# Kernel tuning notes

Measured on AMD Instinct MI355X. Metric: run time of the kernel, lower is better.

Reference implementation:

```python
import jax, jax.numpy as jnp
import numpy as np

H = 128          # hidden_dim
L = 3            # n_layers
G = 128          # num graphs in batch
BN_EPS = 1e-5


def setup_inputs() -> dict:
    key = jax.random.key(0)
    ks = jax.random.split(key, 16)
    N, E, ND, ED = 2048, 8192, 32, 16
    s = lambda k, shape, fan: jax.random.normal(k, shape, dtype=jnp.float32) / np.sqrt(fan)
    return {
        "x": jax.random.normal(ks[0], (N, ND), dtype=jnp.float32),
        "edge_index": jax.random.randint(ks[1], (2, E), 0, N),
        "edge_attr": jax.random.normal(ks[2], (E, ED), dtype=jnp.float32),
        "batch": jnp.sort(jax.random.randint(ks[3], (N,), 0, G)),
        "node_W": s(ks[4], (ND, H), ND),
        "node_b": jnp.zeros((H,), jnp.float32),
        "edge_W": s(ks[5], (L, ED, H * H), ED),
        "edge_b": jnp.zeros((L, H * H), jnp.float32),
        "root_W": s(ks[6], (L, H, H), H),
        "conv_bias": jnp.zeros((L, H), jnp.float32),
        "bn_gamma": jnp.ones((L, H), jnp.float32),
        "bn_beta": jnp.zeros((L, H), jnp.float32),
        "cls_W1": s(ks[7], (H, 64), H),
        "cls_b1": jnp.zeros((64,), jnp.float32),
        "cls_W2": s(ks[8], (64, 1), 64),
        "cls_b2": jnp.zeros((1,), jnp.float32),
    }


def _segment_mean(vals, ids, num_segments):
    ssum = jax.ops.segment_sum(vals, ids, num_segments=num_segments)
    cnt = jax.ops.segment_sum(jnp.ones((vals.shape[0],), vals.dtype), ids,
                              num_segments=num_segments)
    return ssum / jnp.maximum(cnt, 1.0)[:, None]


def reference(x, edge_index, edge_attr, batch, node_W, node_b, edge_W, edge_b,
              root_W, conv_bias, bn_gamma, bn_beta, cls_W1, cls_b1, cls_W2, cls_b2):
    N = x.shape[0]
    src, dst = edge_index[0], edge_index[1]
    h = x @ node_W + node_b                                   # [N, H]
    for l in range(L):
        # edge-conditioned weights: [E, H, H]
        W = (edge_attr @ edge_W[l] + edge_b[l]).reshape(-1, H, H)
        msg = jnp.einsum('ei,eio->eo', h[src], W)             # gather + per-edge matmul
        agg = _segment_mean(msg, dst, N)                      # scatter-mean
        x_new = h @ root_W[l] + agg + conv_bias[l]
        # BatchNorm (batch statistics, training-mode math)
        mu = jnp.mean(x_new, axis=0)
        var = jnp.var(x_new, axis=0)
        x_new = (x_new - mu) * jax.lax.rsqrt(var + BN_EPS) * bn_gamma[l] + bn_beta[l]
        x_new = jax.nn.relu(x_new)                            # dropout omitted (eval)
        h = h + x_new                                         # residual
    g = _segment_mean(h, batch, G)                            # global mean pool [G, H]
    out = jax.nn.relu(g @ cls_W1 + cls_b1) @ cls_W2 + cls_b2  # classifier
    return out.squeeze(-1)                                    # [G]
```

## Files before the change

kernel.cpp:

```cpp
#include <hip/hip_runtime.h>
#include <cstddef>
#include <cstdint>

#define H 128
#define EDIM 16
#define NLAYER 3
#define KU 2304
#define NSLICE 18
#define ASTRIDE 2312

typedef unsigned short ushort_t;
typedef unsigned int uint_t;
typedef __attribute__((ext_vector_type(8))) short bf16x8;
typedef __attribute__((ext_vector_type(4))) float f32x4;

__device__ __forceinline__ ushort_t f2bf(float f) {
    uint_t u = __builtin_bit_cast(uint_t, f);
    u += 0x7fffu + ((u >> 16) & 1u);
    return (ushort_t)(u >> 16);
}
__device__ __forceinline__ uint_t pack2(float a, float b) {
    return (uint_t)f2bf(a) | ((uint_t)f2bf(b) << 16);
}

__global__ __launch_bounds__(1024) void setup_kernel(
    const int* __restrict__ dst, const int* __restrict__ batch,
    const float* __restrict__ x, const float* __restrict__ node_W,
    const float* __restrict__ node_b,
    const float* __restrict__ eW, const float* __restrict__ eb,
    const float* __restrict__ rW,
    int* __restrict__ offs, int* __restrict__ deg, int* __restrict__ eord,
    float* __restrict__ cntG, float* __restrict__ bnS, float* __restrict__ bnQ,
    float* __restrict__ gsum, float* __restrict__ h, ushort_t* __restrict__ Wt2,
    int E, int N, int G)
{
    alignas(16) __shared__ unsigned char smem[36864];
    const int b = blockIdx.x;
    const int t = threadIdx.x;

    if (b == 0) {
        int* sh = (int*)smem;
        int* part = sh + 2048;
        for (int i = t; i < N; i += 1024) sh[i] = 0;
        __syncthreads();
        for (int e = t; e < E; e += 1024) atomicAdd(&sh[dst[e]], 1);
        __syncthreads();
        const int v0 = (2 * t < N) ? sh[2 * t] : 0;
        const int v1 = (2 * t + 1 < N) ? sh[2 * t + 1] : 0;
        part[t] = v0 + v1;
        __syncthreads();
        for (int off = 1; off < 1024; off <<= 1) {
            int xp = (t >= off) ? part[t - off] : 0;
            __syncthreads();
            part[t] += xp;
            __syncthreads();
        }
        const int boff = (t == 0) ? 0 : part[t - 1];
        if (2 * t < N) { deg[2 * t] = v0; offs[2 * t] = boff; }
        if (2 * t + 1 < N) { deg[2 * t + 1] = v1; offs[2 * t + 1] = boff + v0; }
        if (t == 1023) offs[N] = part[1023];
        __syncthreads();
        if (2 * t < N) sh[2 * t] = boff;
        if (2 * t + 1 < N) sh[2 * t + 1] = boff + v0;
        __syncthreads();
        for (int e = t; e < E; e += 1024) {
            const int d = dst[e];
            const int pos = atomicAdd(&sh[d], 1);
            eord[pos] = e;
        }
        return;
    }

    if (b <= NLAYER * NSLICE) {
        ushort_t* tile = (ushort_t*)smem;
        const int bb = b - 1;
        const int l = bb / NSLICE, s = bb % NSLICE;
        const float* S = (s < 16) ? (eW + ((size_t)l * 16 + s) * (H * H))
                       : (s == 16 ? (eb + (size_t)l * H * H)
                                  : (rW + (size_t)l * H * H));
        const int k = t >> 3, o0 = (t & 7) * 16;
#pragma unroll
        for (int j = 0; j < 16; j += 4) {
            float4 v = *(const float4*)&S[(size_t)k * H + o0 + j];
            tile[k * 136 + o0 + j + 0] = f2bf(v.x);
            tile[k * 136 + o0 + j + 1] = f2bf(v.y);
            tile[k * 136 + o0 + j + 2] = f2bf(v.z);
            tile[k * 136 + o0 + j + 3] = f2bf(v.w);
        }
        __syncthreads();
        const int n = t >> 3, k0 = (t & 7) * 16;
        ushort_t* outp = Wt2 + ((size_t)(l * H + n)) * KU + s * H + k0;
#pragma unroll
        for (int j = 0; j < 16; ++j) outp[j] = tile[(k0 + j) * 136 + n];
        return;
    }

    if (b <= NLAYER * NSLICE + 16) {
        const int sub = t >> 8;
        const int st = t & 255;
        float* As = (float*)(smem + sub * 8704);
        float* Bs = As + 16 * 68;
        const int tt = (b - (NLAYER * NSLICE + 1)) * 4 + sub;
        const int bm = (tt >> 1) * 64;
        const int bn = (tt & 1) * 64;
        const int tx = st & 15, ty = st >> 4;
        float acc[4][4];
#pragma unroll
        for (int i = 0; i < 4; ++i)
#pragma unroll
            for (int j = 0; j < 4; ++j) acc[i][j] = 0.f;
        const int ka = st & 15, ma = st >> 4;
        const int nb = st & 63, kb = st >> 6;
        for (int k0 = 0; k0 < 32; k0 += 16) {
#pragma unroll
            for (int r = 0; r < 4; ++r)
                As[ka * 68 + ma + 16 * r] = x[(size_t)(bm + ma + 16 * r) * 32 + (k0 + ka)];
#pragma unroll
            for (int r = 0; r < 4; ++r)
                Bs[(kb + 4 * r) * 68 + nb] = node_W[(size_t)(k0 + kb + 4 * r) * H + bn + nb];
            __syncthreads();
#pragma unroll
            for (int kk = 0; kk < 16; ++kk) {
                const float4 a4 = *(const float4*)&As[kk * 68 + ty * 4];
                const float4 b4 = *(const float4*)&Bs[kk * 68 + tx * 4];
                const float a[4] = {a4.x, a4.y, a4.z, a4.w};
                const float bv[4] = {b4.x, b4.y, b4.z, b4.w};
#pragma unroll
                for (int i = 0; i < 4; ++i)
#pragma unroll
                    for (int j = 0; j < 4; ++j)
                        acc[i][j] = fmaf(a[i], bv[j], acc[i][j]);
            }
            __syncthreads();
        }
#pragma unroll
        for (int i = 0; i < 4; ++i) {
            const int row = bm + ty * 4 + i;
            float4 v;
            v.x = acc[i][0] + node_b[bn + tx * 4 + 0];
            v.y = acc[i][1] + node_b[bn + tx * 4 + 1];
            v.z = acc[i][2] + node_b[bn + tx * 4 + 2];
            v.w = acc[i][3] + node_b[bn + tx * 4 + 3];
            *(float4*)&h[(size_t)row * H + bn + tx * 4] = v;
        }
        return;
    }

    {
        const int zcount = G * H + 2 * NLAYER * H + G;
        for (int i = t; i < zcount; i += 1024) {
            if (i < G * H) gsum[i] = 0.f;
            else if (i < G * H + NLAYER * H) bnS[i - G * H] = 0.f;
            else if (i < G * H + 2 * NLAYER * H) bnQ[i - G * H - NLAYER * H] = 0.f;
            else cntG[i - G * H - 2 * NLAYER * H] = 0.f;
        }
        __syncthreads();
        for (int v = t; v < N; v += 1024) atomicAdd(&cntG[batch[v]], 1.f);
    }
}

__global__ __launch_bounds__(512, 4) void ubuild_gemm(
    const float* __restrict__ h, const float* __restrict__ ea,
    const int* __restrict__ src, const int* __restrict__ offs,
    const int* __restrict__ deg, const int* __restrict__ eord,
    const ushort_t* __restrict__ Wt2l,
    float* __restrict__ xnew, float* __restrict__ bnS, float* __restrict__ bnQ)
{
    __shared__ ushort_t As8[8 * ASTRIDE];
    __shared__ ushort_t Bs[128][136];
    const int tid = threadIdx.x;
    const int w = tid >> 6;
    const int lane = tid & 63;
    const int m0 = blockIdx.x * 8;

    {
        const int v = m0 + w;
        const int j = lane;
        float u[17][2];
#pragma unroll
        for (int d = 0; d < 17; ++d) { u[d][0] = 0.f; u[d][1] = 0.f; }
        const int st = offs[v];
        const int dg = deg[v];
        for (int k = 0; k < dg; ++k) {
            const int e = eord[st + k];
            const int s = src[e];
            const float* eap = ea + (size_t)e * EDIM;
            const float4 w0 = *(const float4*)(eap + 0);
            const float4 w1 = *(const float4*)(eap + 4);
            const float4 w2 = *(const float4*)(eap + 8);
            const float4 w3 = *(const float4*)(eap + 12);
            const float wv[16] = {w0.x, w0.y, w0.z, w0.w, w1.x, w1.y, w1.z, w1.w,
                                  w2.x, w2.y, w2.z, w2.w, w3.x, w3.y, w3.z, w3.w};
            const float2 h2 = *(const float2*)&h[(size_t)s * H + 2 * j];
            u[16][0] += h2.x;
            u[16][1] += h2.y;
#pragma unroll
            for (int d = 0; d < 16; ++d) {
                u[d][0] = fmaf(wv[d], h2.x, u[d][0]);
                u[d][1] = fmaf(wv[d], h2.y, u[d][1]);
            }
        }
        const float rc = 1.0f / (float)(dg > 0 ? dg : 1);
        uint_t* urow = (uint_t*)&As8[w * ASTRIDE];
#pragma unroll
        for (int d = 0; d < 17; ++d)
            urow[j + d * 64] = pack2(u[d][0] * rc, u[d][1] * rc);
        const float2 hv = *(const float2*)&h[(size_t)v * H + 2 * j];
        urow[j + 17 * 64] = pack2(hv.x, hv.y);
    }

    const int l15 = lane & 15, quad = lane >> 4;
    f32x4 acc = {0.f, 0.f, 0.f, 0.f};
    const ushort_t* arow = &As8[(l15 & 7) * ASTRIDE];

    for (int c = 0; c < KU / 128; ++c) {
#pragma unroll
        for (int r = 0; r < 4; ++r) {
            const int idx = tid + r * 512;
            const int row = idx >> 4, pos = (idx & 15) * 8;
            *(uint4*)&Bs[row][pos] =
                *(const uint4*)&Wt2l[(size_t)row * KU + c * 128 + pos];
        }
        __syncthreads();
#pragma unroll
        for (int ks = 0; ks < 4; ++ks) {
            const int k = ks * 32 + quad * 8;
            bf16x8 a = *(const bf16x8*)&arow[c * 128 + k];
            bf16x8 b = *(const bf16x8*)&Bs[w * 16 + l15][k];
            acc = __builtin_amdgcn_mfma_f32_16x16x32_bf16(a, b, acc, 0, 0, 0);
        }
        __syncthreads();
    }

    const int col = w * 16 + l15;
    float s = 0.f, q = 0.f;
    if (quad < 2) {
#pragma unroll
        for (int r = 0; r < 4; ++r) {
            const int m = quad * 4 + r;
            const float val = acc[r];
            xnew[(size_t)(m0 + m) * H + col] = val;
            s += val;
            q += val * val;
        }
    }
    s += __shfl_down(s, 16);
    q += __shfl_down(q, 16);
    if (lane < 16) {
        atomicAdd(&bnS[col], s);
        atomicAdd(&bnQ[col], q);
    }
}

__global__ __launch_bounds__(256) void bn_apply(
    float* __restrict__ h, const float* __restrict__ xnew,
    const float* __restrict__ bnS, const float* __restrict__ bnQ,
    const float* __restrict__ gamma, const float* __restrict__ beta,
    const int* __restrict__ batch, float* __restrict__ gsum, int N, int last)
{
    const int idx = blockIdx.x * 256 + threadIdx.x;
    const int c = idx & 127;
    const int v = idx >> 7;
    const float invN = 1.0f / (float)N;
    const float mu = bnS[c] * invN;
    const float var = bnQ[c] * invN - mu * mu;
    const float val = (xnew[idx] - mu) * rsqrtf(var + 1e-5f) * gamma[c] + beta[c];
    const float hn = h[idx] + fmaxf(val, 0.f);
    h[idx] = hn;
    if (last) atomicAdd(&gsum[batch[v] * H + c], hn);
}

__global__ void classifier_kernel(
    const float* __restrict__ gsum, const float* __restrict__ cntG,
    const float* __restrict__ W1, const float* __restrict__ b1,
    const float* __restrict__ W2, const float* __restrict__ b2,
    float* __restrict__ out)
{
    const int g = blockIdx.x;
    const int j = threadIdx.x;
    const float rc = 1.0f / fmaxf(cntG[g], 1.0f);
    float acc = b1[j];
#pragma unroll 8
    for (int i = 0; i < H; ++i)
        acc = fmaf(gsum[g * H + i] * rc, W1[i * 64 + j], acc);
    float pv = fmaxf(acc, 0.f) * W2[j];
#pragma unroll
    for (int off = 32; off > 0; off >>= 1)
        pv += __shfl_down(pv, off);
    if (j == 0) out[g] = pv + b2[0];
}

extern "C" void kernel_launch(void* const* d_in, const int* in_sizes, int n_in,
                              void* d_out, int out_size, void* d_ws, size_t ws_size,
                              hipStream_t stream)
{
    const float* x      = (const float*)d_in[0];
    const int*   eidx   = (const int*)  d_in[1];
    const float* eattr  = (const float*)d_in[2];
    const int*   batch  = (const int*)  d_in[3];
    const float* node_W = (const float*)d_in[4];
    const float* node_b = (const float*)d_in[5];
    const float* edge_W = (const float*)d_in[6];
    const float* edge_b = (const float*)d_in[7];
    const float* root_W = (const float*)d_in[8];
    const float* gamma  = (const float*)d_in[10];
    const float* beta   = (const float*)d_in[11];
    const float* W1     = (const float*)d_in[12];
    const float* b1     = (const float*)d_in[13];
    const float* W2     = (const float*)d_in[14];
    const float* b2     = (const float*)d_in[15];
    float* out = (float*)d_out;

    const int N = in_sizes[0] / 32;
    const int E = in_sizes[1] / 2;
    const int G = out_size;

    const int* src = eidx;
    const int* dst = eidx + E;

    int* offs  = (int*)d_ws;
    int* deg   = offs + (N + 16);
    int* eord  = deg + N;
    float* cntG = (float*)(eord + E);
    float* bnS  = cntG + G;
    float* bnQ  = bnS + NLAYER * H;
    float* gsum = bnQ + NLAYER * H;
    float* h    = gsum + (size_t)G * H;
    float* xnew = h + (size_t)N * H;
    ushort_t* Wt2 = (ushort_t*)(xnew + (size_t)N * H);

    const int nsetup = 1 + NLAYER * NSLICE + 16 + 1;

    setup_kernel<<<nsetup, 1024, 0, stream>>>(
        dst, batch, x, node_W, node_b, edge_W, edge_b, root_W,
        offs, deg, eord, cntG, bnS, bnQ, gsum, h, Wt2, E, N, G);

    for (int l = 0; l < NLAYER; ++l) {
        ubuild_gemm<<<N / 8, 512, 0, stream>>>(
            h, eattr, src, offs, deg, eord,
            Wt2 + (size_t)l * H * KU,
            xnew, bnS + l * H, bnQ + l * H);
        bn_apply<<<(N * H) / 256, 256, 0, stream>>>(
            h, xnew, bnS + l * H, bnQ + l * H,
            gamma + (size_t)l * H, beta + (size_t)l * H,
            batch, gsum, N, l == NLAYER - 1);
    }

    classifier_kernel<<<G, 64, 0, stream>>>(gsum, cntG, W1, b1, W2, b2, out);
}
```

Before: 206.5 us.

## Fuse all stages into one persistent kernel with software grid barriers

Merges setup, the per-layer message-build GEMM, the batch-norm apply and the classifier into a single persistent kernel of 256 blocks. The stages are separated by atomic grid-wide barriers instead of separate kernel launches. Setup work is redistributed across 512-thread blocks, and the node projection becomes a simple per-thread dot product. This removes several launch gaps and inter-kernel drains, at the cost of relying on all 256 blocks being co-resident for the spin barriers, plus barrier latency and a memset launch.

```diff
diff --git a/kernel.cpp b/kernel.cpp
--- a/kernel.cpp
+++ b/kernel.cpp
@@ -8,6 +8,8 @@
 #define KU 2304
 #define NSLICE 18
 #define ASTRIDE 2312
+#define NB 256
+#define TH 512
 
 typedef unsigned short ushort_t;
 typedef unsigned int uint_t;
@@ -23,64 +25,93 @@
     return (uint_t)f2bf(a) | ((uint_t)f2bf(b) << 16);
 }
 
-__global__ __launch_bounds__(1024) void setup_kernel(
-    const int* __restrict__ dst, const int* __restrict__ batch,
-    const float* __restrict__ x, const float* __restrict__ node_W,
-    const float* __restrict__ node_b,
-    const float* __restrict__ eW, const float* __restrict__ eb,
-    const float* __restrict__ rW,
-    int* __restrict__ offs, int* __restrict__ deg, int* __restrict__ eord,
-    float* __restrict__ cntG, float* __restrict__ bnS, float* __restrict__ bnQ,
-    float* __restrict__ gsum, float* __restrict__ h, ushort_t* __restrict__ Wt2,
-    int E, int N, int G)
+struct MP {
+    const float *x, *eattr, *node_W, *node_b, *edge_W, *edge_b, *root_W;
+    const float *gamma, *beta, *W1, *b1, *W2, *b2;
+    const int *src, *dst, *batch;
+    int *bar;
+    int *offs, *deg, *eord;
+    float *cntG, *bnS, *bnQ, *gsum, *h, *xnew, *out;
+    ushort_t *Wt2;
+    int E, N, G;
+};
+
+__device__ __forceinline__ void gbar(int* cnt, int* gen, int mygen)
 {
-    alignas(16) __shared__ unsigned char smem[36864];
+    __syncthreads();
+    if (threadIdx.x == 0) {
+        __threadfence();
+        int prev = __hip_atomic_fetch_add(cnt, 1, __ATOMIC_ACQ_REL,
+                                          __HIP_MEMORY_SCOPE_AGENT);
+        if (prev == NB - 1) {
+            __hip_atomic_store(cnt, 0, __ATOMIC_RELAXED, __HIP_MEMORY_SCOPE_AGENT);
+            __hip_atomic_store(gen, mygen, __ATOMIC_RELEASE, __HIP_MEMORY_SCOPE_AGENT);
+        } else {
+            while (__hip_atomic_load(gen, __ATOMIC_ACQUIRE,
+                                     __HIP_MEMORY_SCOPE_AGENT) < mygen)
+                __builtin_amdgcn_s_sleep(2);
+        }
+        __threadfence();
+    }
+    __syncthreads();
+}
+
+__global__ __launch_bounds__(TH) void mega(MP p)
+{
+    alignas(16) __shared__ unsigned char smem[71808];
     const int b = blockIdx.x;
     const int t = threadIdx.x;
+    const int N = p.N, E = p.E, G = p.G;
 
     if (b == 0) {
         int* sh = (int*)smem;
         int* part = sh + 2048;
-        for (int i = t; i < N; i += 1024) sh[i] = 0;
-        __syncthreads();
-        for (int e = t; e < E; e += 1024) atomicAdd(&sh[dst[e]], 1);
-        __syncthreads();
-        const int v0 = (2 * t < N) ? sh[2 * t] : 0;
-        const int v1 = (2 * t + 1 < N) ? sh[2 * t + 1] : 0;
-        part[t] = v0 + v1;
-        __syncthreads();
-        for (int off = 1; off < 1024; off <<= 1) {
+        for (int i = t; i < N; i += TH) sh[i] = 0;
+        __syncthreads();
+        for (int e = t; e < E; e += TH) atomicAdd(&sh[p.dst[e]], 1);
+        __syncthreads();
+        const int base = t * 4;
+        int v[4], loc[4], s = 0;
+#pragma unroll
+        for (int j = 0; j < 4; ++j) v[j] = (base + j < N) ? sh[base + j] : 0;
+#pragma unroll
+        for (int j = 0; j < 4; ++j) { loc[j] = s; s += v[j]; }
+        part[t] = s;
+        __syncthreads();
+        for (int off = 1; off < TH; off <<= 1) {
             int xp = (t >= off) ? part[t - off] : 0;
             __syncthreads();
             part[t] += xp;
             __syncthreads();
         }
         const int boff = (t == 0) ? 0 : part[t - 1];
-        if (2 * t < N) { deg[2 * t] = v0; offs[2 * t] = boff; }
-        if (2 * t + 1 < N) { deg[2 * t + 1] = v1; offs[2 * t + 1] = boff + v0; }
-        if (t == 1023) offs[N] = part[1023];
-        __syncthreads();
-        if (2 * t < N) sh[2 * t] = boff;
-        if (2 * t + 1 < N) sh[2 * t + 1] = boff + v0;
-        __syncthreads();
-        for (int e = t; e < E; e += 1024) {
-            const int d = dst[e];
+#pragma unroll
+        for (int j = 0; j < 4; ++j) {
+            if (base + j < N) {
+                p.deg[base + j] = v[j];
+                p.offs[base + j] = boff + loc[j];
+            }
+        }
+        __syncthreads();
+#pragma unroll
+        for (int j = 0; j < 4; ++j)
+            if (base + j < N) sh[base + j] = boff + loc[j];
+        __syncthreads();
+        for (int e = t; e < E; e += TH) {
+            const int d = p.dst[e];
             const int pos = atomicAdd(&sh[d], 1);
-            eord[pos] = e;
-        }
-        return;
-    }
-
-    if (b <= NLAYER * NSLICE) {
+            p.eord[pos] = e;
+        }
+    } else if (b >= 2 && b < 2 + NLAYER * NSLICE) {
         ushort_t* tile = (ushort_t*)smem;
-        const int bb = b - 1;
+        const int bb = b - 2;
         const int l = bb / NSLICE, s = bb % NSLICE;
-        const float* S = (s < 16) ? (eW + ((size_t)l * 16 + s) * (H * H))
-                       : (s == 16 ? (eb + (size_t)l * H * H)
-                                  : (rW + (size_t)l * H * H));
-        const int k = t >> 3, o0 = (t & 7) * 16;
-#pragma unroll
-        for (int j = 0; j < 16; j += 4) {
+        const float* S = (s < 16) ? (p.edge_W + ((size_t)l * 16 + s) * (H * H))
+                       : (s == 16 ? (p.edge_b + (size_t)l * H * H)
+                                  : (p.root_W + (size_t)l * H * H));
+        const int k = t >> 2, o0 = (t & 3) * 32;
+#pragma unroll
+        for (int j = 0; j < 32; j += 4) {
             float4 v = *(const float4*)&S[(size_t)k * H + o0 + j];
             tile[k * 136 + o0 + j + 0] = f2bf(v.x);
             tile[k * 136 + o0 + j + 1] = f2bf(v.y);
@@ -88,263 +119,202 @@
             tile[k * 136 + o0 + j + 3] = f2bf(v.w);
         }
         __syncthreads();
-        const int n = t >> 3, k0 = (t & 7) * 16;
-        ushort_t* outp = Wt2 + ((size_t)(l * H + n)) * KU + s * H + k0;
-#pragma unroll
-        for (int j = 0; j < 16; ++j) outp[j] = tile[(k0 + j) * 136 + n];
-        return;
+        const int n = t >> 2, k0 = (t & 3) * 32;
+        ushort_t* outp = p.Wt2 + ((size_t)(l * H + n)) * KU + s * H + k0;
+#pragma unroll
+        for (int j = 0; j < 32; ++j) outp[j] = tile[(k0 + j) * 136 + n];
+    } else if (b >= 64 && b < 96) {
+        const int m0 = (b - 64) * 64;
+        for (int it = 0; it < 16; ++it) {
+            const int idx = it * TH + t;
+            const int row = m0 + (idx >> 7), col = idx & 127;
+            float acc = p.node_b[col];
+#pragma unroll 8
+            for (int k = 0; k < 32; ++k)
+                acc = fmaf(p.x[(size_t)row * 32 + k], p.node_W[k * H + col], acc);
+            p.h[(size_t)row * H + col] = acc;
+        }
+    } else if (b == 56) {
+        int* c = (int*)smem;
+        for (int i = t; i < G; i += TH) c[i] = 0;
+        __syncthreads();
+        for (int v = t; v < N; v += TH) atomicAdd(&c[p.batch[v]], 1);
+        __syncthreads();
+        for (int i = t; i < G; i += TH) p.cntG[i] = (float)c[i];
+    } else if (b == 57) {
+        for (int i = t; i < G * H; i += TH) p.gsum[i] = 0.f;
+    } else if (b == 58) {
+        for (int i = t; i < 2 * NLAYER * H; i += TH) {
+            if (i < NLAYER * H) p.bnS[i] = 0.f;
+            else p.bnQ[i - NLAYER * H] = 0.f;
+        }
     }
-
-    if (b <= NLAYER * NSLICE + 16) {
-        const int sub = t >> 8;
-        const int st = t & 255;
-        float* As = (float*)(smem + sub * 8704);
-        float* Bs = As + 16 * 68;
-        const int tt = (b - (NLAYER * NSLICE + 1)) * 4 + sub;
-        const int bm = (tt >> 1) * 64;
-        const int bn = (tt & 1) * 64;
-        const int tx = st & 15, ty = st >> 4;
-        float acc[4][4];
-#pragma unroll
-        for (int i = 0; i < 4; ++i)
-#pragma unroll
-            for (int j = 0; j < 4; ++j) acc[i][j] = 0.f;
-        const int ka = st & 15, ma = st >> 4;
-        const int nb = st & 63, kb = st >> 6;
-        for (int k0 = 0; k0 < 32; k0 += 16) {
-#pragma unroll
-            for (int r = 0; r < 4; ++r)
-                As[ka * 68 + ma + 16 * r] = x[(size_t)(bm + ma + 16 * r) * 32 + (k0 + ka)];
-#pragma unroll
-            for (int r = 0; r < 4; ++r)
-                Bs[(kb + 4 * r) * 68 + nb] = node_W[(size_t)(k0 + kb + 4 * r) * H + bn + nb];
+    gbar(p.bar, p.bar + 1, 1);
+
+    ushort_t* As8 = (ushort_t*)smem;
+    ushort_t* Bs = (ushort_t*)(smem + 8 * ASTRIDE * 2);
+    const int m0 = b * 8;
+    const int w = t >> 6;
+    const int lane = t & 63;
+    const int l15 = lane & 15, quad = lane >> 4;
+
+    for (int l = 0; l < NLAYER; ++l) {
+        const ushort_t* Wt2l = p.Wt2 + (size_t)l * H * KU;
+
+        {
+            const int v = m0 + w;
+            const int j = lane;
+            float u[17][2];
+#pragma unroll
+            for (int d = 0; d < 17; ++d) { u[d][0] = 0.f; u[d][1] = 0.f; }
+            const int st = p.offs[v];
+            const int dg = p.deg[v];
+            for (int k = 0; k < dg; ++k) {
+                const int e = p.eord[st + k];
+                const int s = p.src[e];
+                const float* eap = p.eattr + (size_t)e * EDIM;
+                const float4 w0 = *(const float4*)(eap + 0);
+                const float4 w1 = *(const float4*)(eap + 4);
+                const float4 w2 = *(const float4*)(eap + 8);
+                const float4 w3 = *(const float4*)(eap + 12);
+                const float wv[16] = {w0.x, w0.y, w0.z, w0.w, w1.x, w1.y, w1.z, w1.w,
+                                      w2.x, w2.y, w2.z, w2.w, w3.x, w3.y, w3.z, w3.w};
+                const float2 h2 = *(const float2*)&p.h[(size_t)s * H + 2 * j];
+                u[16][0] += h2.x;
+                u[16][1] += h2.y;
+#pragma unroll
+                for (int d = 0; d < 16; ++d) {
+                    u[d][0] = fmaf(wv[d], h2.x, u[d][0]);
+                    u[d][1] = fmaf(wv[d], h2.y, u[d][1]);
+                }
+            }
+            const float rc = 1.0f / (float)(dg > 0 ? dg : 1);
+            uint_t* urow = (uint_t*)&As8[w * ASTRIDE];
+#pragma unroll
+            for (int d = 0; d < 17; ++d)
+                urow[j + d * 64] = pack2(u[d][0] * rc, u[d][1] * rc);
+            const float2 hv = *(const float2*)&p.h[(size_t)v * H + 2 * j];
+            urow[j + 17 * 64] = pack2(hv.x, hv.y);
+        }
+
+        f32x4 acc = {0.f, 0.f, 0.f, 0.f};
+        const ushort_t* arow = &As8[(l15 & 7) * ASTRIDE];
+        for (int c = 0; c < KU / 128; ++c) {
+#pragma unroll
+            for (int r = 0; r < 4; ++r) {
+                const int idx = t + r * TH;
+                const int row = idx >> 4, pos = (idx & 15) * 8;
+                *(uint4*)&Bs[row * 136 + pos] =
+                    *(const uint4*)&Wt2l[(size_t)row * KU + c * 128 + pos];
+            }
             __syncthreads();
 #pragma unroll
-            for (int kk = 0; kk < 16; ++kk) {
-                const float4 a4 = *(const float4*)&As[kk * 68 + ty * 4];
-                const float4 b4 = *(const float4*)&Bs[kk * 68 + tx * 4];
-                const float a[4] = {a4.x, a4.y, a4.z, a4.w};
-                const float bv[4] = {b4.x, b4.y, b4.z, b4.w};
-#pragma unroll
-                for (int i = 0; i < 4; ++i)
-#pragma unroll
-                    for (int j = 0; j < 4; ++j)
-                        acc[i][j] = fmaf(a[i], bv[j], acc[i][j]);
+            for (int ks = 0; ks < 4; ++ks) {
+                const int k = ks * 32 + quad * 8;
+                bf16x8 a = *(const bf16x8*)&arow[c * 128 + k];
+                bf16x8 bb = *(const bf16x8*)&Bs[(w * 16 + l15) * 136 + k];
+                acc = __builtin_amdgcn_mfma_f32_16x16x32_bf16(a, bb, acc, 0, 0, 0);
             }
             __syncthreads();
         }
-#pragma unroll
-        for (int i = 0; i < 4; ++i) {
-            const int row = bm + ty * 4 + i;
-            float4 v;
-            v.x = acc[i][0] + node_b[bn + tx * 4 + 0];
-            v.y = acc[i][1] + node_b[bn + tx * 4 + 1];
-            v.z = acc[i][2] + node_b[bn + tx * 4 + 2];
-            v.w = acc[i][3] + node_b[bn + tx * 4 + 3];
-            *(float4*)&h[(size_t)row * H + bn + tx * 4] = v;
-        }
-        return;
+
+        const int col = w * 16 + l15;
+        float s = 0.f, q = 0.f;
+        if (quad < 2) {
+#pragma unroll
+            for (int r = 0; r < 4; ++r) {
+                const int m = quad * 4 + r;
+                const float val = acc[r];
+                p.xnew[(size_t)(m0 + m) * H + col] = val;
+                s += val;
+                q += val * val;
+            }
+        }
+        s += __shfl_down(s, 16);
+        q += __shfl_down(q, 16);
+        if (lane < 16) {
+            atomicAdd(&p.bnS[l * H + col], s);
+            atomicAdd(&p.bnQ[l * H + col], q);
+        }
+        gbar(p.bar, p.bar + 1, 2 + 2 * l);
+
+        {
+            const float invN = 1.0f / (float)N;
+            const int last = (l == NLAYER - 1);
+            for (int i = t; i < 8 * H; i += TH) {
+                const int v = m0 + (i >> 7);
+                const int c = i & 127;
+                const int idx = v * H + c;
+                const float mu = p.bnS[l * H + c] * invN;
+                const float var = p.bnQ[l * H + c] * invN - mu * mu;
+                const float val = (p.xnew[idx] - mu) * rsqrtf(var + 1e-5f)
+                                * p.gamma[l * H + c] + p.beta[l * H + c];
+                const float hn = p.h[idx] + fmaxf(val, 0.f);
+                p.h[idx] = hn;
+                if (last) atomicAdd(&p.gsum[p.batch[v] * H + c], hn);
+            }
+        }
+        gbar(p.bar, p.bar + 1, 3 + 2 * l);
     }
 
-    {
-        const int zcount = G * H + 2 * NLAYER * H + G;
-        for (int i = t; i < zcount; i += 1024) {
-            if (i < G * H) gsum[i] = 0.f;
-            else if (i < G * H + NLAYER * H) bnS[i - G * H] = 0.f;
-            else if (i < G * H + 2 * NLAYER * H) bnQ[i - G * H - NLAYER * H] = 0.f;
-            else cntG[i - G * H - 2 * NLAYER * H] = 0.f;
-        }
-        __syncthreads();
-        for (int v = t; v < N; v += 1024) atomicAdd(&cntG[batch[v]], 1.f);
+    if (b < G && t < 64) {
+        const int g = b;
+        const int j = t;
+        const float rc = 1.0f / fmaxf(p.cntG[g], 1.0f);
+        float acc = p.b1[j];
+#pragma unroll 8
+        for (int i = 0; i < H; ++i)
+            acc = fmaf(p.gsum[g * H + i] * rc, p.W1[i * 64 + j], acc);
+        float pv = fmaxf(acc, 0.f) * p.W2[j];
+#pragma unroll
+        for (int off = 32; off > 0; off >>= 1)
+            pv += __shfl_down(pv, off);
+        if (j == 0) p.out[g] = pv + p.b2[0];
     }
-}
-
-__global__ __launch_bounds__(512, 4) void ubuild_gemm(
-    const float* __restrict__ h, const float* __restrict__ ea,
-    const int* __restrict__ src, const int* __restrict__ offs,
-    const int* __restrict__ deg, const int* __restrict__ eord,
-    const ushort_t* __restrict__ Wt2l,
-    float* __restrict__ xnew, float* __restrict__ bnS, float* __restrict__ bnQ)
-{
-    __shared__ ushort_t As8[8 * ASTRIDE];
-    __shared__ ushort_t Bs[128][136];
-    const int tid = threadIdx.x;
-    const int w = tid >> 6;
-    const int lane = tid & 63;
-    const int m0 = blockIdx.x * 8;
-
-    {
-        const int v = m0 + w;
-        const int j = lane;
-        float u[17][2];
-#pragma unroll
-        for (int d = 0; d < 17; ++d) { u[d][0] = 0.f; u[d][1] = 0.f; }
-        const int st = offs[v];
-        const int dg = deg[v];
-        for (int k = 0; k < dg; ++k) {
-            const int e = eord[st + k];
-            const int s = src[e];
-            const float* eap = ea + (size_t)e * EDIM;
-            const float4 w0 = *(const float4*)(eap + 0);
-            const float4 w1 = *(const float4*)(eap + 4);
-            const float4 w2 = *(const float4*)(eap + 8);
-            const float4 w3 = *(const float4*)(eap + 12);
-            const float wv[16] = {w0.x, w0.y, w0.z, w0.w, w1.x, w1.y, w1.z, w1.w,
-                                  w2.x, w2.y, w2.z, w2.w, w3.x, w3.y, w3.z, w3.w};
-            const float2 h2 = *(const float2*)&h[(size_t)s * H + 2 * j];
-            u[16][0] += h2.x;
-            u[16][1] += h2.y;
-#pragma unroll
-            for (int d = 0; d < 16; ++d) {
-                u[d][0] = fmaf(wv[d], h2.x, u[d][0]);
-                u[d][1] = fmaf(wv[d], h2.y, u[d][1]);
-            }
-        }
-        const float rc = 1.0f / (float)(dg > 0 ? dg : 1);
-        uint_t* urow = (uint_t*)&As8[w * ASTRIDE];
-#pragma unroll
-        for (int d = 0; d < 17; ++d)
-            urow[j + d * 64] = pack2(u[d][0] * rc, u[d][1] * rc);
-        const float2 hv = *(const float2*)&h[(size_t)v * H + 2 * j];
-        urow[j + 17 * 64] = pack2(hv.x, hv.y);
-    }
-
-    const int l15 = lane & 15, quad = lane >> 4;
-    f32x4 acc = {0.f, 0.f, 0.f, 0.f};
-    const ushort_t* arow = &As8[(l15 & 7) * ASTRIDE];
-
-    for (int c = 0; c < KU / 128; ++c) {
-#pragma unroll
-        for (int r = 0; r < 4; ++r) {
-            const int idx = tid + r * 512;
-            const int row = idx >> 4, pos = (idx & 15) * 8;
-            *(uint4*)&Bs[row][pos] =
-                *(const uint4*)&Wt2l[(size_t)row * KU + c * 128 + pos];
-        }
-        __syncthreads();
-#pragma unroll
-        for (int ks = 0; ks < 4; ++ks) {
-            const int k = ks * 32 + quad * 8;
-            bf16x8 a = *(const bf16x8*)&arow[c * 128 + k];
-            bf16x8 b = *(const bf16x8*)&Bs[w * 16 + l15][k];
-            acc = __builtin_amdgcn_mfma_f32_16x16x32_bf16(a, b, acc, 0, 0, 0);
-        }
-        __syncthreads();
-    }
-
-    const int col = w * 16 + l15;
-    float s = 0.f, q = 0.f;
-    if (quad < 2) {
-#pragma unroll
-        for (int r = 0; r < 4; ++r) {
-            const int m = quad * 4 + r;
-            const float val = acc[r];
-            xnew[(size_t)(m0 + m) * H + col] = val;
-            s += val;
-            q += val * val;
-        }
-    }
-    s += __shfl_down(s, 16);
-    q += __shfl_down(q, 16);
-    if (lane < 16) {
-        atomicAdd(&bnS[col], s);
-        atomicAdd(&bnQ[col], q);
-    }
-}
-
-__global__ __launch_bounds__(256) void bn_apply(
-    float* __restrict__ h, const float* __restrict__ xnew,
-    const float* __restrict__ bnS, const float* __restrict__ bnQ,
-    const float* __restrict__ gamma, const float* __restrict__ beta,
-    const int* __restrict__ batch, float* __restrict__ gsum, int N, int last)
-{
-    const int idx = blockIdx.x * 256 + threadIdx.x;
-    const int c = idx & 127;
-    const int v = idx >> 7;
-    const float invN = 1.0f / (float)N;
-    const float mu = bnS[c] * invN;
-    const float var = bnQ[c] * invN - mu * mu;
-    const float val = (xnew[idx] - mu) * rsqrtf(var + 1e-5f) * gamma[c] + beta[c];
-    const float hn = h[idx] + fmaxf(val, 0.f);
-    h[idx] = hn;
-    if (last) atomicAdd(&gsum[batch[v] * H + c], hn);
-}
-
-__global__ void classifier_kernel(
-    const float* __restrict__ gsum, const float* __restrict__ cntG,
-    const float* __restrict__ W1, const float* __restrict__ b1,
-    const float* __restrict__ W2, const float* __restrict__ b2,
-    float* __restrict__ out)
-{
-    const int g = blockIdx.x;
-    const int j = threadIdx.x;
-    const float rc = 1.0f / fmaxf(cntG[g], 1.0f);
-    float acc = b1[j];
-#pragma unroll 8
-    for (int i = 0; i < H; ++i)
-        acc = fmaf(gsum[g * H + i] * rc, W1[i * 64 + j], acc);
-    float pv = fmaxf(acc, 0.f) * W2[j];
-#pragma unroll
-    for (int off = 32; off > 0; off >>= 1)
-        pv += __shfl_down(pv, off);
-    if (j == 0) out[g] = pv + b2[0];
 }
 
 extern "C" void kernel_launch(void* const* d_in, const int* in_sizes, int n_in,
                               void* d_out, int out_size, void* d_ws, size_t ws_size,
                               hipStream_t stream)
 {
-    const float* x      = (const float*)d_in[0];
-    const int*   eidx   = (const int*)  d_in[1];
-    const float* eattr  = (const float*)d_in[2];
-    const int*   batch  = (const int*)  d_in[3];
-    const float* node_W = (const float*)d_in[4];
-    const float* node_b = (const float*)d_in[5];
-    const float* edge_W = (const float*)d_in[6];
-    const float* edge_b = (const float*)d_in[7];
-    const float* root_W = (const float*)d_in[8];
-    const float* gamma  = (const float*)d_in[10];
-    const float* beta   = (const float*)d_in[11];
-    const float* W1     = (const float*)d_in[12];
-    const float* b1     = (const float*)d_in[13];
-    const float* W2     = (const float*)d_in[14];
-    const float* b2     = (const float*)d_in[15];
-    float* out = (float*)d_out;
-
-    const int N = in_sizes[0] / 32;
-    const int E = in_sizes[1] / 2;
-    const int G = out_size;
-
-    const int* src = eidx;
-    const int* dst = eidx + E;
-
-    int* offs  = (int*)d_ws;
-    int* deg   = offs + (N + 16);
-    int* eord  = deg + N;
-    float* cntG = (float*)(eord + E);
-    float* bnS  = cntG + G;
-    float* bnQ  = bnS + NLAYER * H;
-    float* gsum = bnQ + NLAYER * H;
-    float* h    = gsum + (size_t)G * H;
-    float* xnew = h + (size_t)N * H;
-    ushort_t* Wt2 = (ushort_t*)(xnew + (size_t)N * H);
-
-    const int nsetup = 1 + NLAYER * NSLICE + 16 + 1;
-
-    setup_kernel<<<nsetup, 1024, 0, stream>>>(
-        dst, batch, x, node_W, node_b, edge_W, edge_b, root_W,
-        offs, deg, eord, cntG, bnS, bnQ, gsum, h, Wt2, E, N, G);
-
-    for (int l = 0; l < NLAYER; ++l) {
-        ubuild_gemm<<<N / 8, 512, 0, stream>>>(
-            h, eattr, src, offs, deg, eord,
-            Wt2 + (size_t)l * H * KU,
-            xnew, bnS + l * H, bnQ + l * H);
-        bn_apply<<<(N * H) / 256, 256, 0, stream>>>(
-            h, xnew, bnS + l * H, bnQ + l * H,
-            gamma + (size_t)l * H, beta + (size_t)l * H,
-            batch, gsum, N, l == NLAYER - 1);
-    }
-
-    classifier_kernel<<<G, 64, 0, stream>>>(gsum, cntG, W1, b1, W2, b2, out);
-}
+    MP p;
+    p.x      = (const float*)d_in[0];
+    const int* eidx = (const int*)d_in[1];
+    p.eattr  = (const float*)d_in[2];
+    p.batch  = (const int*)  d_in[3];
+    p.node_W = (const float*)d_in[4];
+    p.node_b = (const float*)d_in[5];
+    p.edge_W = (const float*)d_in[6];
+    p.edge_b = (const float*)d_in[7];
+    p.root_W = (const float*)d_in[8];
+    p.gamma  = (const float*)d_in[10];
+    p.beta   = (const float*)d_in[11];
+    p.W1     = (const float*)d_in[12];
+    p.b1     = (const float*)d_in[13];
+    p.W2     = (const float*)d_in[14];
+    p.b2     = (const float*)d_in[15];
+    p.out    = (float*)d_out;
+
+    p.N = in_sizes[0] / 32;
+    p.E = in_sizes[1] / 2;
+    p.G = out_size;
+    p.src = eidx;
+    p.dst = eidx + p.E;
+
+    const int N = p.N, E = p.E, G = p.G;
+
+    p.bar  = (int*)d_ws;
+    p.offs = p.bar + 4;
+    p.deg  = p.offs + (N + 16);
+    p.eord = p.deg + N;
+    p.cntG = (float*)(p.eord + E);
+    p.bnS  = p.cntG + G;
+    p.bnQ  = p.bnS + NLAYER * H;
+    p.gsum = p.bnQ + NLAYER * H;
+    p.h    = p.gsum + (size_t)G * H;
+    p.xnew = p.h + (size_t)N * H;
+    p.Wt2  = (ushort_t*)(p.xnew + (size_t)N * H);
+
+    hipMemsetAsync(p.bar, 0, 16, stream);
+    mega<<<NB, TH, 0, stream>>>(p);
+}
```

Result: slower. 476.4 us (+130.7%).
